# Kernel tuning notes

Hardware: AMD Instinct MI355X
Metric: run time of the kernel (lower is better)

Reference implementation:

```python
import jax, jax.numpy as jnp
import numpy as np

B, S, D, H = 4, 2048, 1024, 16
DK = D // H


def setup_inputs() -> dict:
    key = jax.random.key(0)
    ks = jax.random.split(key, 12)
    std = 0.02
    inp = {
        "query": jax.random.normal(ks[0], (B, S, D), jnp.float32),
        "key": jax.random.normal(ks[1], (B, S, D), jnp.float32),
        "value": jax.random.normal(ks[2], (B, S, D), jnp.float32),
        "mask": jnp.ones((B, 1, 1, S), jnp.int32),
        "Wq": jax.random.normal(ks[3], (D, D), jnp.float32) * std,
        "bq": jnp.zeros((D,), jnp.float32),
        "Wk": jax.random.normal(ks[4], (D, D), jnp.float32) * std,
        "bk": jnp.zeros((D,), jnp.float32),
        "Wv": jax.random.normal(ks[5], (D, D), jnp.float32) * std,
        "bv": jnp.zeros((D,), jnp.float32),
        "Wo": jax.random.normal(ks[6], (D, D), jnp.float32) * std,
        "bo": jnp.zeros((D,), jnp.float32),
    }
    return inp


def reference(query, key, value, mask, Wq, bq, Wk, bk, Wv, bv, Wo, bo):
    # nn.Linear: x @ W.T + b; then split heads -> [B, H, S, DK]
    def proj(x, W, b):
        y = x @ W.T + b
        return y.reshape(B, S, H, DK).transpose(0, 2, 1, 3)

    q = proj(query, Wq, bq)
    k = proj(key, Wk, bk)
    v = proj(value, Wv, bv)

    scale = 1.0 / jnp.sqrt(jnp.asarray(DK, q.dtype))
    scores = jnp.einsum('bhqd,bhkd->bhqk', q, k) * scale  # [B,H,S,S]
    scores = jnp.where(mask == 0, jnp.asarray(-1e9, scores.dtype), scores)
    p_attn = jax.nn.softmax(scores, axis=-1)  # dropout p=0 -> identity
    ctx = jnp.einsum('bhqk,bhkd->bhqd', p_attn, v)
    ctx = ctx.transpose(0, 2, 1, 3).reshape(B, S, D)
    out = ctx @ Wo.T + bo
    return out
```

## Files before the change

kernel.cpp:

```cpp
#include <hip/hip_runtime.h>

#define BB 4
#define SS 2048
#define DD 1024
#define HH 16
#define DKC 64
#define MT (BB*SS)

typedef _Float16 f16x8 __attribute__((ext_vector_type(8)));
typedef _Float16 f16x4 __attribute__((ext_vector_type(4)));
typedef float f32x4 __attribute__((ext_vector_type(4)));

typedef __attribute__((address_space(1))) void GV;
typedef __attribute__((address_space(3))) void LV;

__device__ __forceinline__ void async_copy16(const void* g, void* l) {
  __builtin_amdgcn_global_load_lds((GV*)g, (LV*)l, 16, 0, 0);
}

__global__ __launch_bounds__(256) void cvt3(const float* __restrict__ s0,
                                            const float* __restrict__ s1,
                                            const float* __restrict__ s2,
                                            _Float16* __restrict__ dst, int n) {
  const float* src = (blockIdx.y == 0) ? s0 : ((blockIdx.y == 1) ? s1 : s2);
  _Float16* d = dst + (size_t)blockIdx.y * n;
  int i = (blockIdx.x * 256 + threadIdx.x) * 4;
  if (i < n) {
    float4 f = *(const float4*)(src + i);
    f16x4 o;
    o[0] = (_Float16)f.x; o[1] = (_Float16)f.y;
    o[2] = (_Float16)f.z; o[3] = (_Float16)f.w;
    *(f16x4*)(d + i) = o;
  }
}

__global__ __launch_bounds__(256) void cvt4(const float* __restrict__ s0,
                                            const float* __restrict__ s1,
                                            const float* __restrict__ s2,
                                            const float* __restrict__ s3,
                                            _Float16* __restrict__ dst, int n) {
  const float* src = (blockIdx.y == 0) ? s0 : ((blockIdx.y == 1) ? s1 :
                     ((blockIdx.y == 2) ? s2 : s3));
  _Float16* d = dst + (size_t)blockIdx.y * n;
  int i = (blockIdx.x * 256 + threadIdx.x) * 4;
  if (i < n) {
    float4 f = *(const float4*)(src + i);
    f16x4 o;
    o[0] = (_Float16)f.x; o[1] = (_Float16)f.y;
    o[2] = (_Float16)f.z; o[3] = (_Float16)f.w;
    *(f16x4*)(d + i) = o;
  }
}

__global__ __launch_bounds__(256) void gemm_qkv(const _Float16* __restrict__ Xb,
                                                const _Float16* __restrict__ Wb,
                                                const float* __restrict__ b0,
                                                const float* __restrict__ b1,
                                                const float* __restrict__ b2,
                                                _Float16* __restrict__ Pj) {
  const int z = blockIdx.z;
  const _Float16* A = Xb + (size_t)z * MT * DD;
  const _Float16* W = Wb + (size_t)z * DD * DD;
  const float* bias = (z == 0) ? b0 : ((z == 1) ? b1 : b2);
  _Float16* out = Pj + (size_t)z * MT * DD;

  const int m0 = blockIdx.y * 128;
  const int n0 = blockIdx.x * 128;
  const int t = threadIdx.x;
  const int lane = t & 63;
  const int wave = t >> 6;
  const int q = lane >> 4, r = lane & 15;
  const int wm = (wave & 1) * 64, wn = (wave >> 1) * 64;

  __shared__ __align__(16) _Float16 sA[128 * 32];
  __shared__ __align__(16) _Float16 sB[128 * 32];

  f32x4 acc[4][4] = {};

  for (int k0 = 0; k0 < DD; k0 += 32) {
#pragma unroll
    for (int i = 0; i < 2; ++i) {
      int c = t + 256 * i;
      int row = c >> 2, cc = c & 3;
      async_copy16(A + (size_t)(m0 + row) * DD + k0 + cc * 8, &sA[c * 8]);
      async_copy16(W + (size_t)(n0 + row) * DD + k0 + cc * 8, &sB[c * 8]);
    }
    __syncthreads();
    f16x8 af[4], bf[4];
#pragma unroll
    for (int x = 0; x < 4; ++x) {
      af[x] = *(const f16x8*)&sA[(wm + x * 16 + r) * 32 + q * 8];
      bf[x] = *(const f16x8*)&sB[(wn + x * 16 + r) * 32 + q * 8];
    }
#pragma unroll
    for (int mi = 0; mi < 4; ++mi)
#pragma unroll
      for (int ni = 0; ni < 4; ++ni)
        acc[mi][ni] = __builtin_amdgcn_mfma_f32_16x16x32_f16(af[mi], bf[ni], acc[mi][ni], 0, 0, 0);
    __syncthreads();
  }

  if (z == 2) {
#pragma unroll
    for (int ni = 0; ni < 4; ++ni) {
      int gn = n0 + wn + ni * 16 + r;
      float bv = bias[gn];
      int h = gn >> 6, dk = gn & 63;
#pragma unroll
      for (int mi = 0; mi < 4; ++mi) {
        int gm = m0 + wm + mi * 16 + q * 4;
        int bb = gm >> 11, s = gm & 2047;
        f16x4 o4;
#pragma unroll
        for (int rr = 0; rr < 4; ++rr) o4[rr] = (_Float16)(acc[mi][ni][rr] + bv);
        *(f16x4*)&out[((size_t)((bb * HH + h) * DKC + dk)) * SS + s] = o4;
      }
    }
  } else {
#pragma unroll
    for (int ni = 0; ni < 4; ++ni) {
      int gn = n0 + wn + ni * 16 + r;
      float bv = bias[gn];
      int h = gn >> 6, dk = gn & 63;
#pragma unroll
      for (int mi = 0; mi < 4; ++mi) {
#pragma unroll
        for (int rr = 0; rr < 4; ++rr) {
          int gm = m0 + wm + mi * 16 + q * 4 + rr;
          int bb = gm >> 11, s = gm & 2047;
          out[((size_t)((bb * HH + h) * SS + s)) * DKC + dk] = (_Float16)(acc[mi][ni][rr] + bv);
        }
      }
    }
  }
}

__global__ __launch_bounds__(256) void attn(const _Float16* __restrict__ Pj,
                                            const int* __restrict__ mask,
                                            _Float16* __restrict__ Cx) {
  const int qt = blockIdx.x, h = blockIdx.y, bb = blockIdx.z;
  const size_t hoff = ((size_t)(bb * HH + h) * SS) * DKC;
  const _Float16* Qh  = Pj + hoff;
  const _Float16* Kh  = Pj + (size_t)MT * DD + hoff;
  const _Float16* Vth = Pj + (size_t)2 * MT * DD + hoff;
  _Float16* Ch = Cx + hoff;
  const int* mrow = mask + bb * SS;

  const int t = threadIdx.x, lane = t & 63, wave = t >> 6;
  const int q = lane >> 4, r = lane & 15;
  const int qrow0 = qt * 128 + wave * 32;

  __shared__ __align__(16) _Float16 sK[64 * 64];
  __shared__ __align__(16) _Float16 sVt[64 * 64];
  __shared__ __align__(16) _Float16 sP[4][32 * 64];

  f16x8 qf[2][2];
#pragma unroll
  for (int mi = 0; mi < 2; ++mi)
#pragma unroll
    for (int kk = 0; kk < 2; ++kk)
      qf[mi][kk] = *(const f16x8*)&Qh[(size_t)(qrow0 + mi * 16 + r) * DKC + kk * 32 + q * 8];

  float lst[2][4] = {};
  f32x4 oacc[2][4] = {};

  const float C2 = 0.125f * 1.44269504089f;

  const int srow0 = t >> 3, scc = t & 7;

  f16x8 kpre[2], vpre[2];
#pragma unroll
  for (int i = 0; i < 2; ++i) {
    int row = srow0 + 32 * i;
    kpre[i] = *(const f16x8*)(Kh + (size_t)row * DKC + scc * 8);
    vpre[i] = *(const f16x8*)(Vth + (size_t)row * SS + scc * 8);
  }

  for (int kt = 0; kt < SS; kt += 64) {
#pragma unroll
    for (int i = 0; i < 2; ++i) {
      int row = srow0 + 32 * i;
      int off = row * 64 + (((scc ^ (row & 7)) << 3));
      *(f16x8*)&sK [off] = kpre[i];
      *(f16x8*)&sVt[off] = vpre[i];
    }
    __syncthreads();

    if (kt + 64 < SS) {
#pragma unroll
      for (int i = 0; i < 2; ++i) {
        int row = srow0 + 32 * i;
        kpre[i] = *(const f16x8*)(Kh + (size_t)(kt + 64 + row) * DKC + scc * 8);
        vpre[i] = *(const f16x8*)(Vth + (size_t)row * SS + kt + 64 + scc * 8);
      }
    }

    f32x4 sacc[2][4] = {};
#pragma unroll
    for (int kk = 0; kk < 2; ++kk) {
      f16x8 kb[4];
#pragma unroll
      for (int ni = 0; ni < 4; ++ni)
        kb[ni] = *(const f16x8*)&sK[(ni * 16 + r) * 64 + ((((kk * 4 + q) ^ (r & 7)) << 3))];
#pragma unroll
      for (int mi = 0; mi < 2; ++mi)
#pragma unroll
        for (int ni = 0; ni < 4; ++ni)
          sacc[mi][ni] = __builtin_amdgcn_mfma_f32_16x16x32_f16(qf[mi][kk], kb[ni], sacc[mi][ni], 0, 0, 0);
    }

    float mb[4];
#pragma unroll
    for (int ni = 0; ni < 4; ++ni) mb[ni] = mrow[kt + ni * 16 + r] ? 0.0f : -1e30f;

#pragma unroll
    for (int mi = 0; mi < 2; ++mi) {
#pragma unroll
      for (int rr = 0; rr < 4; ++rr) {
        int rowoff = (mi * 16 + q * 4 + rr) * 64;
        int ksw = ((q << 1) | (rr & 1)) << 3;
#pragma unroll
        for (int ni = 0; ni < 4; ++ni) {
          float p = __builtin_amdgcn_exp2f(__builtin_fmaf(sacc[mi][ni][rr], C2, mb[ni]));
          lst[mi][rr] += p;
          sP[wave][rowoff + ((ni * 16 + r) ^ ksw)] = (_Float16)p;
        }
      }
    }
    __threadfence_block();

#pragma unroll
    for (int kk = 0; kk < 2; ++kk) {
      f16x8 ap[2], vb[4];
#pragma unroll
      for (int mi = 0; mi < 2; ++mi) {
        int row = mi * 16 + r;
        int ksw = ((((r >> 2) & 3) << 1) | (r & 1)) << 3;
        ap[mi] = *(const f16x8*)&sP[wave][row * 64 + ((kk * 32 + q * 8) ^ ksw)];
      }
#pragma unroll
      for (int ni = 0; ni < 4; ++ni) {
        vb[ni] = *(const f16x8*)&sVt[(ni * 16 + r) * 64 + ((((kk * 4 + q) ^ (r & 7)) << 3))];
      }
#pragma unroll
      for (int mi = 0; mi < 2; ++mi)
#pragma unroll
        for (int ni = 0; ni < 4; ++ni)
          oacc[mi][ni] = __builtin_amdgcn_mfma_f32_16x16x32_f16(ap[mi], vb[ni], oacc[mi][ni], 0, 0, 0);
    }
    __syncthreads();
  }

#pragma unroll
  for (int mi = 0; mi < 2; ++mi)
#pragma unroll
    for (int rr = 0; rr < 4; ++rr) {
      float l = lst[mi][rr];
#pragma unroll
      for (int d = 1; d < 16; d <<= 1) l += __shfl_xor(l, d);
      lst[mi][rr] = 1.0f / l;
    }

#pragma unroll
  for (int mi = 0; mi < 2; ++mi)
#pragma unroll
    for (int ni = 0; ni < 4; ++ni)
#pragma unroll
      for (int rr = 0; rr < 4; ++rr) {
        int row = qrow0 + mi * 16 + q * 4 + rr;
        Ch[(size_t)row * DKC + ni * 16 + r] = (_Float16)(oacc[mi][ni][rr] * lst[mi][rr]);
      }
}

__global__ __launch_bounds__(256) void gemm_out(const _Float16* __restrict__ Cx,
                                                const _Float16* __restrict__ W,
                                                const float* __restrict__ bias,
                                                float* __restrict__ out) {
  const int m0 = blockIdx.y * 128;
  const int n0 = blockIdx.x * 128;
  const int t = threadIdx.x;
  const int lane = t & 63;
  const int wave = t >> 6;
  const int q = lane >> 4, r = lane & 15;
  const int wm = (wave & 1) * 64, wn = (wave >> 1) * 64;

  __shared__ __align__(16) _Float16 sA[128 * 32];
  __shared__ __align__(16) _Float16 sB[128 * 32];

  f32x4 acc[4][4] = {};

  for (int k0 = 0; k0 < DD; k0 += 32) {
#pragma unroll
    for (int i = 0; i < 2; ++i) {
      int c = t + 256 * i;
      int row = c >> 2, cc = c & 3;
      int gm = m0 + row;
      int bb = gm >> 11, s = gm & 2047;
      int head = k0 >> 6, off = (k0 & 63) + cc * 8;
      async_copy16(Cx + ((size_t)(bb * HH + head) * SS + s) * DKC + off, &sA[c * 8]);
      async_copy16(W + (size_t)(n0 + row) * DD + k0 + cc * 8, &sB[c * 8]);
    }
    __syncthreads();
    f16x8 af[4], bf[4];
#pragma unroll
    for (int x = 0; x < 4; ++x) {
      af[x] = *(const f16x8*)&sA[(wm + x * 16 + r) * 32 + q * 8];
      bf[x] = *(const f16x8*)&sB[(wn + x * 16 + r) * 32 + q * 8];
    }
#pragma unroll
    for (int mi = 0; mi < 4; ++mi)
#pragma unroll
      for (int ni = 0; ni < 4; ++ni)
        acc[mi][ni] = __builtin_amdgcn_mfma_f32_16x16x32_f16(af[mi], bf[ni], acc[mi][ni], 0, 0, 0);
    __syncthreads();
  }

#pragma unroll
  for (int ni = 0; ni < 4; ++ni) {
    int gn = n0 + wn + ni * 16 + r;
    float bv = bias[gn];
#pragma unroll
    for (int mi = 0; mi < 4; ++mi) {
#pragma unroll
      for (int rr = 0; rr < 4; ++rr) {
        int gm = m0 + wm + mi * 16 + q * 4 + rr;
        out[(size_t)gm * DD + gn] = acc[mi][ni][rr] + bv;
      }
    }
  }
}

extern "C" void kernel_launch(void* const* d_in, const int* in_sizes, int n_in,
                              void* d_out, int out_size, void* d_ws, size_t ws_size,
                              hipStream_t stream) {
  const float* query = (const float*)d_in[0];
  const float* key_  = (const float*)d_in[1];
  const float* value = (const float*)d_in[2];
  const int*   mask  = (const int*)d_in[3];
  const float* Wq = (const float*)d_in[4];
  const float* bq = (const float*)d_in[5];
  const float* Wk = (const float*)d_in[6];
  const float* bk = (const float*)d_in[7];
  const float* Wv = (const float*)d_in[8];
  const float* bv = (const float*)d_in[9];
  const float* Wo = (const float*)d_in[10];
  const float* bo = (const float*)d_in[11];
  float* out = (float*)d_out;

  const int nX = MT * DD;
  const int nW = DD * DD;

  _Float16* Xb = (_Float16*)d_ws;
  _Float16* Wb = Xb + (size_t)3 * nX;
  _Float16* Pj = Wb + (size_t)4 * nW;
  _Float16* Cx = Pj + (size_t)3 * nX;

  cvt3<<<dim3(nX / 1024, 3), 256, 0, stream>>>(query, key_, value, Xb, nX);
  cvt4<<<dim3(nW / 1024, 4), 256, 0, stream>>>(Wq, Wk, Wv, Wo, Wb, nW);

  gemm_qkv<<<dim3(DD / 128, MT / 128, 3), 256, 0, stream>>>(Xb, Wb, bq, bk, bv, Pj);
  attn<<<dim3(SS / 128, HH, BB), 256, 0, stream>>>(Pj, mask, Cx);
  gemm_out<<<dim3(DD / 128, MT / 128), 256, 0, stream>>>(Cx, Wb + (size_t)3 * nW, bo, out);
}
```

Measured before the change: 415.9 us.

## Fuse fp32-to-fp16 activation conversion into QKV GEMM and cache mask bias in LDS

Removes the separate conversion kernel for query/key/value. The QKV GEMM now loads fp32 activations into registers, prefetches the next K-slice, converts to fp16 and stores into shared memory itself, which avoids writing and re-reading an fp16 copy of the inputs. The cost is that the A tile no longer uses async global-to-LDS copies, and each A tile is re-read as fp32 by every N-block. The attention kernel also precomputes the additive mask bias for the whole sequence into shared memory once per block, instead of reading global mask values every key tile.

```diff
diff --git a/kernel.cpp b/kernel.cpp
--- a/kernel.cpp
+++ b/kernel.cpp
@@ -10,28 +10,13 @@
 typedef _Float16 f16x8 __attribute__((ext_vector_type(8)));
 typedef _Float16 f16x4 __attribute__((ext_vector_type(4)));
 typedef float f32x4 __attribute__((ext_vector_type(4)));
+typedef int   i32x4 __attribute__((ext_vector_type(4)));
 
 typedef __attribute__((address_space(1))) void GV;
 typedef __attribute__((address_space(3))) void LV;
 
 __device__ __forceinline__ void async_copy16(const void* g, void* l) {
   __builtin_amdgcn_global_load_lds((GV*)g, (LV*)l, 16, 0, 0);
-}
-
-__global__ __launch_bounds__(256) void cvt3(const float* __restrict__ s0,
-                                            const float* __restrict__ s1,
-                                            const float* __restrict__ s2,
-                                            _Float16* __restrict__ dst, int n) {
-  const float* src = (blockIdx.y == 0) ? s0 : ((blockIdx.y == 1) ? s1 : s2);
-  _Float16* d = dst + (size_t)blockIdx.y * n;
-  int i = (blockIdx.x * 256 + threadIdx.x) * 4;
-  if (i < n) {
-    float4 f = *(const float4*)(src + i);
-    f16x4 o;
-    o[0] = (_Float16)f.x; o[1] = (_Float16)f.y;
-    o[2] = (_Float16)f.z; o[3] = (_Float16)f.w;
-    *(f16x4*)(d + i) = o;
-  }
 }
 
 __global__ __launch_bounds__(256) void cvt4(const float* __restrict__ s0,
@@ -44,22 +29,24 @@
   _Float16* d = dst + (size_t)blockIdx.y * n;
   int i = (blockIdx.x * 256 + threadIdx.x) * 4;
   if (i < n) {
-    float4 f = *(const float4*)(src + i);
+    f32x4 f = *(const f32x4*)(src + i);
     f16x4 o;
-    o[0] = (_Float16)f.x; o[1] = (_Float16)f.y;
-    o[2] = (_Float16)f.z; o[3] = (_Float16)f.w;
+#pragma unroll
+    for (int j = 0; j < 4; ++j) o[j] = (_Float16)f[j];
     *(f16x4*)(d + i) = o;
   }
 }
 
-__global__ __launch_bounds__(256) void gemm_qkv(const _Float16* __restrict__ Xb,
+__global__ __launch_bounds__(256) void gemm_qkv(const float* __restrict__ Xq,
+                                                const float* __restrict__ Xk,
+                                                const float* __restrict__ Xv,
                                                 const _Float16* __restrict__ Wb,
                                                 const float* __restrict__ b0,
                                                 const float* __restrict__ b1,
                                                 const float* __restrict__ b2,
                                                 _Float16* __restrict__ Pj) {
   const int z = blockIdx.z;
-  const _Float16* A = Xb + (size_t)z * MT * DD;
+  const float* A = (z == 0) ? Xq : ((z == 1) ? Xk : Xv);
   const _Float16* W = Wb + (size_t)z * DD * DD;
   const float* bias = (z == 0) ? b0 : ((z == 1) ? b1 : b2);
   _Float16* out = Pj + (size_t)z * MT * DD;
@@ -77,15 +64,40 @@
 
   f32x4 acc[4][4] = {};
 
+  const int arow = t >> 2, acc_ = t & 3;
+  const float* abase = A + (size_t)(m0 + arow) * DD + acc_ * 8;
+
+  f32x4 apre[2][2];
+#pragma unroll
+  for (int i = 0; i < 2; ++i) {
+    const float* ap = abase + (size_t)(32 * i) * DD;
+    ap = A + (size_t)(m0 + arow + 64 * i) * DD + acc_ * 8;
+    apre[i][0] = *(const f32x4*)ap;
+    apre[i][1] = *(const f32x4*)(ap + 4);
+  }
+
   for (int k0 = 0; k0 < DD; k0 += 32) {
 #pragma unroll
     for (int i = 0; i < 2; ++i) {
       int c = t + 256 * i;
+      f16x8 o;
+#pragma unroll
+      for (int j = 0; j < 4; ++j) { o[j] = (_Float16)apre[i][0][j]; o[j + 4] = (_Float16)apre[i][1][j]; }
+      *(f16x8*)&sA[c * 8] = o;
       int row = c >> 2, cc = c & 3;
-      async_copy16(A + (size_t)(m0 + row) * DD + k0 + cc * 8, &sA[c * 8]);
       async_copy16(W + (size_t)(n0 + row) * DD + k0 + cc * 8, &sB[c * 8]);
     }
     __syncthreads();
+
+    if (k0 + 32 < DD) {
+#pragma unroll
+      for (int i = 0; i < 2; ++i) {
+        const float* ap = A + (size_t)(m0 + arow + 64 * i) * DD + k0 + 32 + acc_ * 8;
+        apre[i][0] = *(const f32x4*)ap;
+        apre[i][1] = *(const f32x4*)(ap + 4);
+      }
+    }
+
     f16x8 af[4], bf[4];
 #pragma unroll
     for (int x = 0; x < 4; ++x) {
@@ -153,6 +165,21 @@
   __shared__ __align__(16) _Float16 sK[64 * 64];
   __shared__ __align__(16) _Float16 sVt[64 * 64];
   __shared__ __align__(16) _Float16 sP[4][32 * 64];
+  __shared__ __align__(16) float    sMB[SS];
+
+  {
+    int i0 = t * 8;
+    i32x4 m0v = *(const i32x4*)(mrow + i0);
+    i32x4 m1v = *(const i32x4*)(mrow + i0 + 4);
+    f32x4 b0v, b1v;
+#pragma unroll
+    for (int j = 0; j < 4; ++j) {
+      b0v[j] = m0v[j] ? 0.0f : -1e30f;
+      b1v[j] = m1v[j] ? 0.0f : -1e30f;
+    }
+    *(f32x4*)&sMB[i0] = b0v;
+    *(f32x4*)&sMB[i0 + 4] = b1v;
+  }
 
   f16x8 qf[2][2];
 #pragma unroll
@@ -211,7 +238,7 @@
 
     float mb[4];
 #pragma unroll
-    for (int ni = 0; ni < 4; ++ni) mb[ni] = mrow[kt + ni * 16 + r] ? 0.0f : -1e30f;
+    for (int ni = 0; ni < 4; ++ni) mb[ni] = sMB[kt + ni * 16 + r];
 
 #pragma unroll
     for (int mi = 0; mi < 2; ++mi) {
@@ -350,15 +377,13 @@
   const int nX = MT * DD;
   const int nW = DD * DD;
 
-  _Float16* Xb = (_Float16*)d_ws;
-  _Float16* Wb = Xb + (size_t)3 * nX;
+  _Float16* Wb = (_Float16*)d_ws;
   _Float16* Pj = Wb + (size_t)4 * nW;
   _Float16* Cx = Pj + (size_t)3 * nX;
 
-  cvt3<<<dim3(nX / 1024, 3), 256, 0, stream>>>(query, key_, value, Xb, nX);
   cvt4<<<dim3(nW / 1024, 4), 256, 0, stream>>>(Wq, Wk, Wv, Wo, Wb, nW);
 
-  gemm_qkv<<<dim3(DD / 128, MT / 128, 3), 256, 0, stream>>>(Xb, Wb, bq, bk, bv, Pj);
+  gemm_qkv<<<dim3(DD / 128, MT / 128, 3), 256, 0, stream>>>(query, key_, value, Wb, bq, bk, bv, Pj);
   attn<<<dim3(SS / 128, HH, BB), 256, 0, stream>>>(Pj, mask, Cx);
   gemm_out<<<dim3(DD / 128, MT / 128), 256, 0, stream>>>(Cx, Wb + (size_t)3 * nW, bo, out);
 }
```

New measurement: 420.4 us. About the same (+1.1%).
